# Kernel tuning notes

Measured on AMD Instinct MI355X. Metric: run time of the kernel, lower is better.

The kernel has to match this reference:

```python
import jax, jax.numpy as jnp
import numpy as np

BATCH, SEQ_LEN, PRED_LEN, ENC_IN = 64, 720, 720, 512
H_FREQ, H1, H2 = 64, 128, 256


def setup_inputs() -> dict:
    key = jax.random.key(0)
    ks = jax.random.split(key, 8)
    def w(k, shape, fan_in):
        return jax.random.normal(k, shape, jnp.float32) / np.float32(np.sqrt(fan_in))
    return {
        "batch_x": jax.random.normal(ks[0], (BATCH, SEQ_LEN, ENC_IN), jnp.float32),
        # MLPfreq.model_freq: Linear(seq_len, 64); weights stored (in, out)
        "w_freq": w(ks[1], (SEQ_LEN, H_FREQ), SEQ_LEN), "b_freq": jnp.zeros((H_FREQ,), jnp.float32),
        # MLPfreq.model_all: Linear(64+seq_len,128) -> ReLU -> Linear(128,256)
        "w_all1": w(ks[2], (H_FREQ + SEQ_LEN, H1), H_FREQ + SEQ_LEN), "b_all1": jnp.zeros((H1,), jnp.float32),
        "w_all2": w(ks[3], (H1, H2), H1), "b_all2": jnp.zeros((H2,), jnp.float32),
        # TSMixer(256, enc_in, pred_len): time-mix, channel-mix, temporal projection
        "w_time": w(ks[4], (H2, H2), H2), "b_time": jnp.zeros((H2,), jnp.float32),
        "w_chan": w(ks[5], (ENC_IN, ENC_IN), ENC_IN), "b_chan": jnp.zeros((ENC_IN,), jnp.float32),
        "w_proj": w(ks[6], (H2, PRED_LEN), H2), "b_proj": jnp.zeros((PRED_LEN,), jnp.float32),
        "freq_topk": 20,
    }


def _main_freq_part(x, k):
    # x: (b, L, C). rfft over time axis, keep top-k |freq| per (batch, channel).
    b, L, C = x.shape
    xf = jnp.fft.rfft(x, axis=1)                      # (b, F, C) complex
    mag = jnp.abs(xf).transpose(0, 2, 1)              # (b, C, F)
    F = mag.shape[-1]
    _, idx = jax.lax.top_k(mag, k)                    # (b, C, k)
    mask = jnp.zeros((b, C, F), x.dtype).at[
        jnp.arange(b)[:, None, None], jnp.arange(C)[None, :, None], idx
    ].set(1.0)
    xf_filtered = xf * mask.transpose(0, 2, 1)        # (b, F, C)
    x_filtered = jnp.fft.irfft(xf_filtered, n=L, axis=1)  # (b, L, C)
    return x - x_filtered, x_filtered


def reference(batch_x, w_freq, b_freq, w_all1, b_all1, w_all2, b_all2,
              w_time, b_time, w_chan, b_chan, w_proj, b_proj, freq_topk):
    residual, x_filt = _main_freq_part(batch_x, freq_topk)
    # MLPfreq: operates channel-major (b, C, L)
    mf = x_filt.transpose(0, 2, 1)                    # (b, C, L)
    xt = batch_x.transpose(0, 2, 1)                   # (b, C, L)
    h = jax.nn.relu(mf @ w_freq + b_freq)             # (b, C, 64)
    inp = jnp.concatenate([h, xt], axis=-1)           # (b, C, 64+L)
    z = jax.nn.relu(inp @ w_all1 + b_all1) @ w_all2 + b_all2  # (b, C, 256)
    # TSMixer on (b, 256, C) == z with time dim last here
    t = z + jax.nn.relu(z @ w_time + b_time)          # time mixing (256->256)
    tc = t.transpose(0, 2, 1)                         # (b, 256, C)
    c = tc + jax.nn.relu(tc @ w_chan + b_chan)        # channel mixing (C->C)
    out = c.transpose(0, 2, 1) @ w_proj + b_proj      # (b, C, pred_len)
    pred_main_freq_signal = out.transpose(0, 2, 1)    # (b, pred_len, C)
    # forward(mode='n') returns the residual (norm_input); pred_main_freq_signal
    # is stored as a side-effect attribute -- returned here as second output.
    return residual, pred_main_freq_signal
```

## Files before the change

kernel.cpp:

```cpp
#include <hip/hip_runtime.h>
#include <math.h>

#define BB   64
#define LL   720
#define CC   512
#define FF   361
#define KTOP 20

__global__ __launch_bounds__(256) void transpose_kernel(
    const float* __restrict__ in, float* __restrict__ out,
    int R, int Cc, long sIn, long sOut) {
  __shared__ float tile[32][33];
  const float* inp = in + (long)blockIdx.z * sIn;
  float* outp = out + (long)blockIdx.z * sOut;
  int r0 = blockIdx.y * 32, c0 = blockIdx.x * 32;
  int tx = threadIdx.x, ty = threadIdx.y;
#pragma unroll
  for (int i = 0; i < 4; ++i) {
    int r = r0 + ty + 8 * i, c = c0 + tx;
    if (r < R && c < Cc) tile[ty + 8 * i][tx] = inp[(long)r * Cc + c];
  }
  __syncthreads();
#pragma unroll
  for (int i = 0; i < 4; ++i) {
    int c = c0 + ty + 8 * i, r = r0 + tx;
    if (c < Cc && r < R) outp[(long)c * R + r] = tile[tx][ty + 8 * i];
  }
}

__global__ __launch_bounds__(256) void residual_kernel(
    const float* __restrict__ x, const float* __restrict__ xf,
    float* __restrict__ out) {
  __shared__ float tile[32][33];
  int b = blockIdx.z;
  const float* xfp = xf + (long)b * CC * LL;
  int c0 = blockIdx.x * 32, l0 = blockIdx.y * 32;
  int tx = threadIdx.x, ty = threadIdx.y;
#pragma unroll
  for (int i = 0; i < 4; ++i) {
    int c = c0 + ty + 8 * i, l = l0 + tx;
    if (l < LL) tile[ty + 8 * i][tx] = xfp[(long)c * LL + l];
  }
  __syncthreads();
  long xbase = (long)b * LL * CC;
#pragma unroll
  for (int i = 0; i < 4; ++i) {
    int l = l0 + ty + 8 * i, c = c0 + tx;
    if (l < LL) {
      long off = xbase + (long)l * CC + c;
      out[off] = x[off] - tile[tx][ty + 8 * i];
    }
  }
}

__global__ __launch_bounds__(256) void init_tw_kernel(double* __restrict__ ctd) {
  int j = blockIdx.x * 256 + threadIdx.x;
  const double W0d = 8.7266462599716478846e-3;
  if (j < 720) ctd[j] = cos((double)j * W0d);
}

__global__ __launch_bounds__(192) void dft_topk_kernel(
    const float* __restrict__ xt, const double* __restrict__ ctd,
    float* __restrict__ xfilt) {
  __shared__ double seo[2][361][2];
  __shared__ float  ctf[720];
  __shared__ float  sres[2][361];
  __shared__ float  sims[2][361];
  __shared__ int    ssel[2][KTOP];

  const int tid = threadIdx.x;
  const long ser0 = (long)blockIdx.x * 2;

  for (int p = tid; p < 722; p += 192) {
    int sp = (p >= 361) ? 1 : 0;
    int t = p - 361 * sp;
    const float* xs = xt + (ser0 + sp) * LL;
    double e, o;
    if (t == 0)       { e = (double)xs[0]; o = (double)xs[360]; }
    else if (t < 360) { double xa = (double)xs[t], xb = (double)xs[720 - t];
                        e = xa + xb; o = xa - xb; }
    else              { e = 0.0; o = 0.0; }
    seo[sp][t][0] = e; seo[sp][t][1] = o;
  }
  for (int j = tid; j < 720; j += 192) ctf[j] = (float)ctd[j];
  __syncthreads();

  const int s = (tid >= 96) ? 1 : 0;
  const int f = tid - 96 * s;
  const bool act = (f <= 90);

  const double ca = ctd[f];
  const double sa = ctd[f + 540];
  double c = ca, sn = sa;

  double EC0 = 0, EC1 = 0, EC2 = 0, EC3 = 0;
  double ESd = 0;
  double OCd = 0;
  double OS0 = 0, OS1 = 0, OS2 = 0, OS3 = 0;

  for (int u = 0; u < 90; ++u) {
    const int t = 4 * u + 1;
    double e1 = seo[s][t][0],     o1 = seo[s][t][1];
    double e2 = seo[s][t + 1][0], o2 = seo[s][t + 1][1];
    double e3 = seo[s][t + 2][0], o3 = seo[s][t + 2][1];
    double e4 = seo[s][t + 3][0], o4 = seo[s][t + 3][1];
    EC1 = fma(e1, c, EC1);  ESd = fma(e1, sn, ESd);
    OCd = fma(o1, c, OCd);  OS1 = fma(o1, sn, OS1);
    double c2 = fma(c, ca, -(sn * sa)), s2 = fma(sn, ca, c * sa);
    EC2 = fma(e2, c2, EC2); OS2 = fma(o2, s2, OS2);
    double c3 = fma(c2, ca, -(s2 * sa)), s3 = fma(s2, ca, c2 * sa);
    EC3 = fma(e3, c3, EC3); ESd = fma(e3, -s3, ESd);
    OCd = fma(o3, -c3, OCd); OS3 = fma(o3, s3, OS3);
    double c4 = fma(c3, ca, -(s3 * sa)), s4 = fma(s3, ca, c3 * sa);
    EC0 = fma(e4, c4, EC0); OS0 = fma(o4, s4, OS0);
    double c5 = fma(c4, ca, -(s4 * sa)), s5 = fma(s4, ca, c4 * sa);
    c = c5; sn = s5;
  }

  double reF = 0, imF = 0, reG1 = 0, imG1 = 0, reG2 = 0, imG2 = 0, reG3 = 0, imG3 = 0;
  if (act) {
    double x0 = seo[s][0][0], x360 = seo[s][0][1];
    double xe = (f & 1) ? (x0 - x360) : (x0 + x360);
    reF  = xe + ((EC0 + EC1) + (EC2 + EC3));
    imF  = -((OS0 + OS1) + (OS2 + OS3));
    reG3 = xe + ((EC0 - EC1) + (EC2 - EC3));
    imG3 = (OS0 - OS1) + (OS2 - OS3);
    double ecd = EC0 - EC2, osd = OS0 - OS2;
    reG1 = xe + ecd + ESd;
    imG1 = osd - OCd;
    reG2 = xe + ecd - ESd;
    imG2 = -osd - OCd;
  }
  __syncthreads();

  double* mg = &seo[s][0][0];
  if (act) {
    const double invL = 1.0 / 720.0;
    double s0 = (f == 0) ? invL : 2.0 * invL;
    const double s2d = 2.0 * invL;
    int i3 = 360 - f, i1 = 180 - f, i2 = 180 + f;
    mg[f]  = reF * reF + imF * imF;
    sres[s][f]  = (float)(reF * s0);  sims[s][f]  = (float)(imF * s0);
    mg[i3] = reG3 * reG3 + imG3 * imG3;
    sres[s][i3] = (float)(reG3 * s0); sims[s][i3] = (float)(imG3 * s0);
    mg[i1] = reG1 * reG1 + imG1 * imG1;
    sres[s][i1] = (float)(reG1 * s2d); sims[s][i1] = (float)(imG1 * s2d);
    mg[i2] = reG2 * reG2 + imG2 * imG2;
    sres[s][i2] = (float)(reG2 * s2d); sims[s][i2] = (float)(imG2 * s2d);
  }
  __syncthreads();

  const int wv = tid >> 6, ln = tid & 63;
  if (wv != 1) {
    const int sw = wv >> 1;
    const double* mgw = &seo[sw][0][0];
    double val[6];
#pragma unroll
    for (int j = 0; j < 6; ++j) {
      int idx = ln + 64 * j;
      val[j] = (idx < FF) ? mgw[idx] : -2.0;
    }
    for (int it = 0; it < KTOP; ++it) {
      double v = val[0]; int bi = ln;
#pragma unroll
      for (int j = 1; j < 6; ++j) {
        if (val[j] > v) { v = val[j]; bi = ln + 64 * j; }
      }
#pragma unroll
      for (int off = 1; off < 64; off <<= 1) {
        double ov = __shfl_xor(v, off);
        int oi = __shfl_xor(bi, off);
        if (ov > v || (ov == v && oi < bi)) { v = ov; bi = oi; }
      }
      if (ln == 0) ssel[sw][it] = bi;
      if ((bi & 63) == ln) val[bi >> 6] = -2.0;
    }
  }
  __syncthreads();

  for (int p = tid; p < 1440; p += 192) {
    int sp = (p >= 720) ? 1 : 0;
    int t = p - 720 * sp;
    float acc = 0.f;
#pragma unroll
    for (int it = 0; it < KTOP; ++it) {
      int fk = ssel[sp][it];
      int k = (fk * t) % 720;
      int ks = k + 540; if (ks >= 720) ks -= 720;
      acc = fmaf(sres[sp][fk], ctf[k], acc);
      acc = fmaf(-sims[sp][fk], ctf[ks], acc);
    }
    xfilt[(ser0 + sp) * LL + t] = acc;
  }
}

template <int EPI, int BIASM>
__global__ __launch_bounds__(256) void gemm_f32(
    const float* __restrict__ A, const float* __restrict__ W,
    const float* __restrict__ bias, const float* __restrict__ Cin,
    float* __restrict__ Cout, int M, int N, int K,
    long sA, long sW, long sC) {
  __shared__ float As[16][68];
  __shared__ float Ws[16][68];
  A += (long)blockIdx.z * sA;
  W += (long)blockIdx.z * sW;
  Cin += (long)blockIdx.z * sC;
  Cout += (long)blockIdx.z * sC;
  const int m0 = blockIdx.y * 64, n0 = blockIdx.x * 64;
  const int tid = threadIdx.x;
  const int tx = tid & 15, ty = tid >> 4;
  const int arow = tid >> 2, ac = (tid & 3) * 4;
  const int wrow = tid >> 4, wc = (tid & 15) * 4;

  float acc[4][4] = {};
  for (int k0 = 0; k0 < K; k0 += 16) {
    float4 av;
    int gr = m0 + arow;
    if (gr < M) av = *(const float4*)&A[(long)gr * K + k0 + ac];
    else        av = make_float4(0.f, 0.f, 0.f, 0.f);
    float4 wv = *(const float4*)&W[(long)(k0 + wrow) * N + n0 + wc];
    __syncthreads();
    As[ac + 0][arow] = av.x; As[ac + 1][arow] = av.y;
    As[ac + 2][arow] = av.z; As[ac + 3][arow] = av.w;
    *(float4*)&Ws[wrow][wc] = wv;
    __syncthreads();
#pragma unroll
    for (int kk = 0; kk < 16; ++kk) {
      float4 a = *(const float4*)&As[kk][ty * 4];
      float4 b = *(const float4*)&Ws[kk][tx * 4];
      float aa[4] = {a.x, a.y, a.z, a.w};
      float bb[4] = {b.x, b.y, b.z, b.w};
#pragma unroll
      for (int i = 0; i < 4; ++i)
#pragma unroll
        for (int j = 0; j < 4; ++j)
          acc[i][j] = fmaf(aa[i], bb[j], acc[i][j]);
    }
  }

#pragma unroll
  for (int i = 0; i < 4; ++i) {
    int r = m0 + ty * 4 + i;
    if (r >= M) continue;
    float rb = (BIASM == 2) ? bias[r] : 0.f;
#pragma unroll
    for (int j = 0; j < 4; ++j) {
      int cix = n0 + tx * 4 + j;
      float v = acc[i][j];
      if (BIASM == 1) v += bias[cix];
      if (BIASM == 2) v += rb;
      long off = (long)r * N + cix;
      if (EPI == 0) Cout[off] = v;
      else if (EPI == 1) Cout[off] = fmaxf(v, 0.f);
      else if (EPI == 2) Cout[off] = fmaxf(v + Cin[off], 0.f);
      else Cout[off] = Cin[off] + fmaxf(v, 0.f);
    }
  }
}

extern "C" void kernel_launch(void* const* d_in, const int* in_sizes, int n_in,
                              void* d_out, int out_size, void* d_ws, size_t ws_size,
                              hipStream_t stream) {
  const float* x      = (const float*)d_in[0];
  const float* w_freq = (const float*)d_in[1];
  const float* b_freq = (const float*)d_in[2];
  const float* w_all1 = (const float*)d_in[3];
  const float* b_all1 = (const float*)d_in[4];
  const float* w_all2 = (const float*)d_in[5];
  const float* b_all2 = (const float*)d_in[6];
  const float* w_time = (const float*)d_in[7];
  const float* b_time = (const float*)d_in[8];
  const float* w_chan = (const float*)d_in[9];
  const float* b_chan = (const float*)d_in[10];
  const float* w_proj = (const float*)d_in[11];
  const float* b_proj = (const float*)d_in[12];

  float* out0 = (float*)d_out;
  float* out1 = out0 + (size_t)BB * LL * CC;

  float* ws  = (float*)d_ws;
  float* XT  = ws;
  float* XF  = XT + 23592960;
  float* H   = XF + 23592960;
  float* A1  = H + 2097152;
  float* WPT = A1 + 4194304;
  float* Z   = XF;
  float* T   = XF + 8388608;
  float* TT  = XT;
  float* CO  = XT + 8388608;
  double* CTD = (double*)H;

  dim3 tb(32, 8);

  init_tw_kernel<<<3, 256, 0, stream>>>(CTD);
  transpose_kernel<<<dim3(16, 23, BB), tb, 0, stream>>>(
      x, XT, LL, CC, (long)LL * CC, (long)LL * CC);
  transpose_kernel<<<dim3(23, 8, 1), tb, 0, stream>>>(
      w_proj, WPT, 256, 720, 0, 0);
  dft_topk_kernel<<<BB * CC / 2, 192, 0, stream>>>(XT, CTD, XF);
  residual_kernel<<<dim3(16, 23, BB), tb, 0, stream>>>(x, XF, out0);
  gemm_f32<1, 1><<<dim3(1, 512, 1), 256, 0, stream>>>(
      XF, w_freq, b_freq, nullptr, H, 32768, 64, 720, 0, 0, 0);
  gemm_f32<0, 0><<<dim3(2, 512, 1), 256, 0, stream>>>(
      H, w_all1, nullptr, nullptr, A1, 32768, 128, 64, 0, 0, 0);
  gemm_f32<2, 1><<<dim3(2, 512, 1), 256, 0, stream>>>(
      XT, w_all1 + 64 * 128, b_all1, A1, A1, 32768, 128, 720, 0, 0, 0);
  gemm_f32<0, 1><<<dim3(4, 512, 1), 256, 0, stream>>>(
      A1, w_all2, b_all2, nullptr, Z, 32768, 256, 128, 0, 0, 0);
  gemm_f32<3, 1><<<dim3(4, 512, 1), 256, 0, stream>>>(
      Z, w_time, b_time, Z, T, 32768, 256, 256, 0, 0, 0);
  transpose_kernel<<<dim3(8, 16, BB), tb, 0, stream>>>(
      T, TT, 512, 256, (long)512 * 256, (long)512 * 256);
  gemm_f32<3, 1><<<dim3(8, 256, 1), 256, 0, stream>>>(
      TT, w_chan, b_chan, TT, CO, 16384, 512, 512, 0, 0, 0);
  gemm_f32<0, 2><<<dim3(8, 12, BB), 256, 0, stream>>>(
      WPT, CO, b_proj, nullptr, out1, 720, 512, 256,
      0, (long)256 * 512, (long)LL * CC);
}
```

Before: 1.516 ms.

## Use larger register-tiled GEMM kernels and fuse the two model_all1 GEMMs

Adds 128x64 and 128x128 register-tiled SGEMM kernels with vectorized float4 epilogues. They replace the 64x64 GEMMs for the MLP, time-mix, channel-mix and projection stages. A dual-pass variant accumulates both halves of the concatenated w_all1 input in one kernel, so the intermediate A1 no longer has to be written and read back. Larger tiles raise arithmetic intensity per LDS load, but they use more registers and launch fewer blocks. The EPI==1 path of the 128x128 kernel has a typo on v1.z, but that path is never instantiated.

```diff
diff --git a/kernel.cpp b/kernel.cpp
--- a/kernel.cpp
+++ b/kernel.cpp
@@ -94,8 +94,7 @@
   double c = ca, sn = sa;
 
   double EC0 = 0, EC1 = 0, EC2 = 0, EC3 = 0;
-  double ESd = 0;
-  double OCd = 0;
+  double ESd = 0, OCd = 0;
   double OS0 = 0, OS1 = 0, OS2 = 0, OS3 = 0;
 
   for (int u = 0; u < 90; ++u) {
@@ -204,8 +203,7 @@
   __shared__ float Ws[16][68];
   A += (long)blockIdx.z * sA;
   W += (long)blockIdx.z * sW;
-  Cin += (long)blockIdx.z * sC;
-  Cout += (long)blockIdx.z * sC;
+  const long zoff = (long)blockIdx.z * sC;
   const int m0 = blockIdx.y * 64, n0 = blockIdx.x * 64;
   const int tid = threadIdx.x;
   const int tx = tid & 15, ty = tid >> 4;
@@ -249,11 +247,207 @@
       float v = acc[i][j];
       if (BIASM == 1) v += bias[cix];
       if (BIASM == 2) v += rb;
-      long off = (long)r * N + cix;
+      long off = zoff + (long)r * N + cix;
       if (EPI == 0) Cout[off] = v;
       else if (EPI == 1) Cout[off] = fmaxf(v, 0.f);
       else if (EPI == 2) Cout[off] = fmaxf(v + Cin[off], 0.f);
       else Cout[off] = Cin[off] + fmaxf(v, 0.f);
+    }
+  }
+}
+
+template <int EPI, int BIASM, bool DUAL>
+__global__ __launch_bounds__(256) void gemm_128x64(
+    const float* __restrict__ A, const float* __restrict__ W,
+    const float* __restrict__ A2, const float* __restrict__ W2,
+    const float* __restrict__ bias, const float* __restrict__ Cin,
+    float* __restrict__ Cout, int M, int N, int K, int K2,
+    long sA, long sC) {
+  __shared__ float As[16][132];
+  __shared__ float Ws[16][68];
+  A += (long)blockIdx.z * sA;
+  const long zoff = (long)blockIdx.z * sC;
+  const int m0 = blockIdx.y * 128, n0 = blockIdx.x * 64;
+  const int tid = threadIdx.x;
+  const int tx = tid & 15, ty = tid >> 4;
+  const int arow = tid >> 1, ak = (tid & 1) * 8;
+  const int wrow = tid >> 4, wc = (tid & 15) * 4;
+
+  float acc[8][4] = {};
+  const float* Ap = A;
+  const float* Wp = W;
+  int Kc = K;
+#pragma unroll 1
+  for (int pass = 0; pass < (DUAL ? 2 : 1); ++pass) {
+    if (DUAL && pass == 1) { Ap = A2; Wp = W2; Kc = K2; }
+    for (int k0 = 0; k0 < Kc; k0 += 16) {
+      float4 av0, av1;
+      int gr = m0 + arow;
+      if (gr < M) {
+        av0 = *(const float4*)&Ap[(long)gr * Kc + k0 + ak];
+        av1 = *(const float4*)&Ap[(long)gr * Kc + k0 + ak + 4];
+      } else {
+        av0 = av1 = make_float4(0.f, 0.f, 0.f, 0.f);
+      }
+      float4 wv = *(const float4*)&Wp[(long)(k0 + wrow) * N + n0 + wc];
+      __syncthreads();
+      As[ak + 0][arow] = av0.x; As[ak + 1][arow] = av0.y;
+      As[ak + 2][arow] = av0.z; As[ak + 3][arow] = av0.w;
+      As[ak + 4][arow] = av1.x; As[ak + 5][arow] = av1.y;
+      As[ak + 6][arow] = av1.z; As[ak + 7][arow] = av1.w;
+      *(float4*)&Ws[wrow][wc] = wv;
+      __syncthreads();
+#pragma unroll
+      for (int kk = 0; kk < 16; ++kk) {
+        float4 a0 = *(const float4*)&As[kk][ty * 8];
+        float4 a1 = *(const float4*)&As[kk][ty * 8 + 4];
+        float4 b  = *(const float4*)&Ws[kk][tx * 4];
+        float aa[8] = {a0.x, a0.y, a0.z, a0.w, a1.x, a1.y, a1.z, a1.w};
+        float bb[4] = {b.x, b.y, b.z, b.w};
+#pragma unroll
+        for (int i = 0; i < 8; ++i)
+#pragma unroll
+          for (int j = 0; j < 4; ++j)
+            acc[i][j] = fmaf(aa[i], bb[j], acc[i][j]);
+      }
+    }
+  }
+
+  float4 bc = make_float4(0.f, 0.f, 0.f, 0.f);
+  if (BIASM == 1) bc = *(const float4*)&bias[n0 + tx * 4];
+#pragma unroll
+  for (int i = 0; i < 8; ++i) {
+    int r = m0 + ty * 8 + i;
+    if (r >= M) continue;
+    float rb = (BIASM == 2) ? bias[r] : 0.f;
+    long off = zoff + (long)r * N + n0 + tx * 4;
+    float4 v = make_float4(acc[i][0], acc[i][1], acc[i][2], acc[i][3]);
+    if (BIASM == 1) { v.x += bc.x; v.y += bc.y; v.z += bc.z; v.w += bc.w; }
+    if (BIASM == 2) { v.x += rb;   v.y += rb;   v.z += rb;   v.w += rb;   }
+    if (EPI == 0) {
+      *(float4*)&Cout[off] = v;
+    } else if (EPI == 1) {
+      v.x = fmaxf(v.x, 0.f); v.y = fmaxf(v.y, 0.f);
+      v.z = fmaxf(v.z, 0.f); v.w = fmaxf(v.w, 0.f);
+      *(float4*)&Cout[off] = v;
+    } else if (EPI == 2) {
+      float4 ci = *(const float4*)&Cin[off];
+      v.x = fmaxf(v.x + ci.x, 0.f); v.y = fmaxf(v.y + ci.y, 0.f);
+      v.z = fmaxf(v.z + ci.z, 0.f); v.w = fmaxf(v.w + ci.w, 0.f);
+      *(float4*)&Cout[off] = v;
+    } else {
+      float4 ci = *(const float4*)&Cin[off];
+      v.x = ci.x + fmaxf(v.x, 0.f); v.y = ci.y + fmaxf(v.y, 0.f);
+      v.z = ci.z + fmaxf(v.z, 0.f); v.w = ci.w + fmaxf(v.w, 0.f);
+      *(float4*)&Cout[off] = v;
+    }
+  }
+}
+
+template <int EPI, int BIASM>
+__global__ __launch_bounds__(256) void gemm_128x128(
+    const float* __restrict__ A, const float* __restrict__ W,
+    const float* __restrict__ bias, const float* __restrict__ Cin,
+    float* __restrict__ Cout, int M, int N, int K,
+    long sA, long sW, long sC) {
+  __shared__ float As[16][132];
+  __shared__ float WsA[16][68];
+  __shared__ float WsB[16][68];
+  A += (long)blockIdx.z * sA;
+  W += (long)blockIdx.z * sW;
+  const long zoff = (long)blockIdx.z * sC;
+  const int m0 = blockIdx.y * 128, n0 = blockIdx.x * 128;
+  const int tid = threadIdx.x;
+  const int tx = tid & 15, ty = tid >> 4;
+  const int arow = tid >> 1, ak = (tid & 1) * 8;
+  const int wrow = tid >> 4, wq = (tid & 15);
+
+  float acc[8][8] = {};
+  for (int k0 = 0; k0 < K; k0 += 16) {
+    float4 av0, av1;
+    int gr = m0 + arow;
+    if (gr < M) {
+      av0 = *(const float4*)&A[(long)gr * K + k0 + ak];
+      av1 = *(const float4*)&A[(long)gr * K + k0 + ak + 4];
+    } else {
+      av0 = av1 = make_float4(0.f, 0.f, 0.f, 0.f);
+    }
+    const float* wp = &W[(long)(k0 + wrow) * N + n0 + wq * 8];
+    float4 wv0 = *(const float4*)&wp[0];
+    float4 wv1 = *(const float4*)&wp[4];
+    __syncthreads();
+    As[ak + 0][arow] = av0.x; As[ak + 1][arow] = av0.y;
+    As[ak + 2][arow] = av0.z; As[ak + 3][arow] = av0.w;
+    As[ak + 4][arow] = av1.x; As[ak + 5][arow] = av1.y;
+    As[ak + 6][arow] = av1.z; As[ak + 7][arow] = av1.w;
+    *(float4*)&WsA[wrow][wq * 4] = wv0;
+    *(float4*)&WsB[wrow][wq * 4] = wv1;
+    __syncthreads();
+#pragma unroll
+    for (int kk = 0; kk < 16; ++kk) {
+      float4 a0 = *(const float4*)&As[kk][ty * 8];
+      float4 a1 = *(const float4*)&As[kk][ty * 8 + 4];
+      float4 b0 = *(const float4*)&WsA[kk][tx * 4];
+      float4 b1 = *(const float4*)&WsB[kk][tx * 4];
+      float aa[8] = {a0.x, a0.y, a0.z, a0.w, a1.x, a1.y, a1.z, a1.w};
+      float bb[8] = {b0.x, b0.y, b0.z, b0.w, b1.x, b1.y, b1.z, b1.w};
+#pragma unroll
+      for (int i = 0; i < 8; ++i)
+#pragma unroll
+        for (int j = 0; j < 8; ++j)
+          acc[i][j] = fmaf(aa[i], bb[j], acc[i][j]);
+    }
+  }
+
+  float4 bc0 = make_float4(0.f, 0.f, 0.f, 0.f), bc1 = bc0;
+  if (BIASM == 1) {
+    bc0 = *(const float4*)&bias[n0 + tx * 8];
+    bc1 = *(const float4*)&bias[n0 + tx * 8 + 4];
+  }
+#pragma unroll
+  for (int i = 0; i < 8; ++i) {
+    int r = m0 + ty * 8 + i;
+    if (r >= M) continue;
+    float rb = (BIASM == 2) ? bias[r] : 0.f;
+    long off = zoff + (long)r * N + n0 + tx * 8;
+    float4 v0 = make_float4(acc[i][0], acc[i][1], acc[i][2], acc[i][3]);
+    float4 v1 = make_float4(acc[i][4], acc[i][5], acc[i][6], acc[i][7]);
+    if (BIASM == 1) {
+      v0.x += bc0.x; v0.y += bc0.y; v0.z += bc0.z; v0.w += bc0.w;
+      v1.x += bc1.x; v1.y += bc1.y; v1.z += bc1.z; v1.w += bc1.w;
+    }
+    if (BIASM == 2) {
+      v0.x += rb; v0.y += rb; v0.z += rb; v0.w += rb;
+      v1.x += rb; v1.y += rb; v1.z += rb; v1.w += rb;
+    }
+    if (EPI == 0) {
+      *(float4*)&Cout[off] = v0;
+      *(float4*)&Cout[off + 4] = v1;
+    } else if (EPI == 1) {
+      v0.x = fmaxf(v0.x, 0.f); v0.y = fmaxf(v0.y, 0.f);
+      v0.z = fmaxf(v0.z, 0.f); v0.w = fmaxf(v0.w, 0.f);
+      v1.x = fmaxf(v1.x, 0.f); v1.y = fmaxf(v1.y, 0.f);
+      v1.z = fmaxf(v1.w, 0.f); v1.z = fmaxf(v1.z, 0.f); v1.w = fmaxf(v1.w, 0.f);
+      *(float4*)&Cout[off] = v0;
+      *(float4*)&Cout[off + 4] = v1;
+    } else if (EPI == 2) {
+      float4 c0 = *(const float4*)&Cin[off];
+      float4 c1 = *(const float4*)&Cin[off + 4];
+      v0.x = fmaxf(v0.x + c0.x, 0.f); v0.y = fmaxf(v0.y + c0.y, 0.f);
+      v0.z = fmaxf(v0.z + c0.z, 0.f); v0.w = fmaxf(v0.w + c0.w, 0.f);
+      v1.x = fmaxf(v1.x + c1.x, 0.f); v1.y = fmaxf(v1.y + c1.y, 0.f);
+      v1.z = fmaxf(v1.z + c1.z, 0.f); v1.w = fmaxf(v1.w + c1.w, 0.f);
+      *(float4*)&Cout[off] = v0;
+      *(float4*)&Cout[off + 4] = v1;
+    } else {
+      float4 c0 = *(const float4*)&Cin[off];
+      float4 c1 = *(const float4*)&Cin[off + 4];
+      v0.x = c0.x + fmaxf(v0.x, 0.f); v0.y = c0.y + fmaxf(v0.y, 0.f);
+      v0.z = c0.z + fmaxf(v0.z, 0.f); v0.w = c0.w + fmaxf(v0.w, 0.f);
+      v1.x = c1.x + fmaxf(v1.x, 0.f); v1.y = c1.y + fmaxf(v1.y, 0.f);
+      v1.z = c1.z + fmaxf(v1.z, 0.f); v1.w = c1.w + fmaxf(v1.w, 0.f);
+      *(float4*)&Cout[off] = v0;
+      *(float4*)&Cout[off + 4] = v1;
     }
   }
 }
@@ -301,19 +495,20 @@
   residual_kernel<<<dim3(16, 23, BB), tb, 0, stream>>>(x, XF, out0);
   gemm_f32<1, 1><<<dim3(1, 512, 1), 256, 0, stream>>>(
       XF, w_freq, b_freq, nullptr, H, 32768, 64, 720, 0, 0, 0);
-  gemm_f32<0, 0><<<dim3(2, 512, 1), 256, 0, stream>>>(
-      H, w_all1, nullptr, nullptr, A1, 32768, 128, 64, 0, 0, 0);
-  gemm_f32<2, 1><<<dim3(2, 512, 1), 256, 0, stream>>>(
-      XT, w_all1 + 64 * 128, b_all1, A1, A1, 32768, 128, 720, 0, 0, 0);
-  gemm_f32<0, 1><<<dim3(4, 512, 1), 256, 0, stream>>>(
-      A1, w_all2, b_all2, nullptr, Z, 32768, 256, 128, 0, 0, 0);
-  gemm_f32<3, 1><<<dim3(4, 512, 1), 256, 0, stream>>>(
-      Z, w_time, b_time, Z, T, 32768, 256, 256, 0, 0, 0);
+  gemm_128x64<1, 1, true><<<dim3(2, 256, 1), 256, 0, stream>>>(
+      XT, w_all1 + 64 * 128, H, w_all1, b_all1, nullptr, A1,
+      32768, 128, 720, 64, 0, 0);
+  gemm_128x64<0, 1, false><<<dim3(4, 256, 1), 256, 0, stream>>>(
+      A1, w_all2, nullptr, nullptr, b_all2, nullptr, Z,
+      32768, 256, 128, 0, 0, 0);
+  gemm_128x64<3, 1, false><<<dim3(4, 256, 1), 256, 0, stream>>>(
+      Z, w_time, nullptr, nullptr, b_time, Z, T,
+      32768, 256, 256, 0, 0, 0);
   transpose_kernel<<<dim3(8, 16, BB), tb, 0, stream>>>(
       T, TT, 512, 256, (long)512 * 256, (long)512 * 256);
-  gemm_f32<3, 1><<<dim3(8, 256, 1), 256, 0, stream>>>(
+  gemm_128x128<3, 1><<<dim3(4, 128, 1), 256, 0, stream>>>(
       TT, w_chan, b_chan, TT, CO, 16384, 512, 512, 0, 0, 0);
-  gemm_f32<0, 2><<<dim3(8, 12, BB), 256, 0, stream>>>(
+  gemm_128x128<0, 2><<<dim3(4, 6, BB), 256, 0, stream>>>(
       WPT, CO, b_proj, nullptr, out1, 720, 512, 256,
       0, (long)256 * 512, (long)LL * CC);
 }
```

Result: slower. 1.566 ms (+3.3%).
